# Performance work log

Hardware: AMD Instinct MI355X
Metric: run time of the kernel (lower is better)

The kernel has to match this reference:

```python
import jax, jax.numpy as jnp
import numpy as np

LEAKY_ALPHA = 0.2      # nn.LeakyReLU(alpha)
NEG_FILL = -9e15       # zero_vec fill value
BN_EPS = 1e-5          # BatchNorm1d default eps

N, F_IN, F_OUT, E = 8192, 256, 64, 262144


def setup_inputs() -> dict:
    key = jax.random.key(0)
    ks = jax.random.split(key, 4)
    h = jax.random.normal(ks[0], (N, F_IN), jnp.float32)
    edge_index = jax.random.randint(ks[1], (2, E), 0, N, dtype=jnp.int64)
    # xavier_uniform-scale params
    W = jax.random.normal(ks[2], (F_IN, F_OUT), jnp.float32) * (1.0 / np.sqrt(F_IN))
    a = jax.random.normal(ks[3], (2 * F_OUT, 1), jnp.float32) * 0.1
    bias = jnp.zeros((F_OUT,), jnp.float32)   # filled with 0.0 in reset_parameters0
    gamma = jnp.ones((F_OUT,), jnp.float32)   # BatchNorm1d weight
    beta = jnp.zeros((F_OUT,), jnp.float32)   # BatchNorm1d bias
    return {"h": h, "edge_index": edge_index, "W": W, "a": a,
            "bias": bias, "gamma": gamma, "beta": beta}


def reference(h, edge_index, W, a, bias, gamma, beta):
    # --- GATLayer (num_heads=1, concat=True, activation=None, dropout off) ---
    hp = h @ W                                   # [N, F_OUT]
    n = hp.shape[0]
    f = hp.shape[1]
    # a_input @ a with a_input[i,j] = [hp_i ; hp_j] decomposes as f1_i + f2_j
    a1, a2 = a[:f, 0], a[f:, 0]
    f1 = hp @ a1                                 # [N]
    f2 = hp @ a2                                 # [N]
    e = jax.nn.leaky_relu(f1[:, None] + f2[None, :], LEAKY_ALPHA)  # [N, N]
    row, col = edge_index[0], edge_index[1]
    adj = jnp.zeros((n, n), dtype=bool).at[row, col].set(True)
    att = jax.nn.softmax(jnp.where(adj, e, NEG_FILL), axis=1)      # [N, N]
    alpha = att[row, col]                        # [E]
    out = att @ hp                               # [N, F_OUT]
    # BatchNorm1d, training mode: batch stats, biased variance
    mean = jnp.mean(out, axis=0)
    var = jnp.mean((out - mean) ** 2, axis=0)
    out = (out - mean) / jnp.sqrt(var + BN_EPS) * gamma + beta
    out = out + bias                             # activation is None
    return out, alpha
```

## Files before the change

kernel.cpp:

```cpp
#include <hip/hip_runtime.h>
#include <stdint.h>

#define N_NODES 8192
#define F_IN    256
#define F_OUT   64
#define N_EDGES 262144
#define LEAKY   0.2f
#define BN_EPSF 1e-5f
#define WPR     256
#define MAXDEG  256
#define WT_LD   260
#define SLOTS   8

typedef unsigned int u32;

__device__ __forceinline__ float lrelu(float x) {
    return fmaxf(x, LEAKY * x);
}

__global__ __launch_bounds__(256) void k_pre(
    const float* __restrict__ h, const float* __restrict__ W, const float* __restrict__ a,
    float* __restrict__ hp, float* __restrict__ f1, float* __restrict__ f2,
    u32* __restrict__ bm, float* __restrict__ Sacc)
{
    __shared__ float Wt[F_OUT * WT_LD];
    const int tid = threadIdx.x;
    const int w = tid >> 6, lane = tid & 63;
    const int b = blockIdx.x;

    {
        const float4 z = {0.f, 0.f, 0.f, 0.f};
        float4* dst = reinterpret_cast<float4*>(bm + (size_t)b * 8192);
#pragma unroll
        for (int p = 0; p < 8; ++p) dst[tid + p * 256] = z;
        if (b == 0 && tid < 256)
            reinterpret_cast<float4*>(Sacc)[tid] = z;
    }

#pragma unroll
    for (int t = 0; t < 64; ++t) {
        const int T = t * 4 + w;
        const int o = (T & 7) * 8 + (lane & 7);
        const int k = (T >> 3) * 8 + (lane >> 3);
        Wt[o * WT_LD + k] = W[k * F_OUT + o];
    }
    __syncthreads();

    const int row0 = b * 32;
    const int wu = __builtin_amdgcn_readfirstlane(w);
    const float* hb = h + (size_t)(row0 + wu * 8) * F_IN;
    const int o = lane;

    float acc[8] = {0.f, 0.f, 0.f, 0.f, 0.f, 0.f, 0.f, 0.f};
    for (int q = 0; q < 64; ++q) {
        const float4 wv = *reinterpret_cast<const float4*>(&Wt[o * WT_LD + 4 * q]);
#pragma unroll
        for (int r = 0; r < 8; ++r) {
            const float4 hq = *reinterpret_cast<const float4*>(&hb[r * F_IN + 4 * q]);
            acc[r] += wv.x * hq.x + wv.y * hq.y + wv.z * hq.z + wv.w * hq.w;
        }
    }

    const float a1 = a[o], a2 = a[F_OUT + o];
#pragma unroll
    for (int r = 0; r < 8; ++r) {
        const int row = row0 + wu * 8 + r;
        hp[row * F_OUT + o] = acc[r];
        float p1 = acc[r] * a1;
        float p2 = acc[r] * a2;
#pragma unroll
        for (int off = 32; off; off >>= 1) {
            p1 += __shfl_xor(p1, off, 64);
            p2 += __shfl_xor(p2, off, 64);
        }
        if (o == 0) { f1[row] = p1; f2[row] = p2; }
    }
}

__global__ __launch_bounds__(256) void k_adj(const int* __restrict__ ei, u32* __restrict__ bm)
{
    const int e = blockIdx.x * 256 + threadIdx.x;
    const int r = ei[e];
    const int c = ei[N_EDGES + e];
    atomicOr(&bm[(size_t)r * WPR + (c >> 5)], 1u << (c & 31));
}

__global__ __launch_bounds__(256) void k_attn(
    const u32* __restrict__ bm, const float* __restrict__ hp,
    const float* __restrict__ f1g, const float* __restrict__ f2g,
    float* __restrict__ Mg, float* __restrict__ Dg, float* __restrict__ outr,
    float* __restrict__ Sacc, float* __restrict__ Qacc)
{
    __shared__ int   nbr[4][MAXDEG];
    __shared__ float fv [4][MAXDEG];
    __shared__ float bnS[4][F_OUT], bnQ[4][F_OUT];
    const int tid = threadIdx.x;
    const int w = tid >> 6, lane = tid & 63;
    const int row = blockIdx.x * 4 + w;

    const uint4 bw = reinterpret_cast<const uint4*>(bm + (size_t)row * WPR)[lane];
    const int tot = __popc(bw.x) + __popc(bw.y) + __popc(bw.z) + __popc(bw.w);
    int pref = tot;
#pragma unroll
    for (int off = 1; off < 64; off <<= 1) {
        const int t2 = __shfl_up(pref, off, 64);
        if (lane >= off) pref += t2;
    }
    const int deg0 = __shfl(pref, 63, 64);
    int pos = pref - tot;
    float mymax = -1e30f;
    const u32 words[4] = {bw.x, bw.y, bw.z, bw.w};
    int* nb = nbr[w];
    float* fvv = fv[w];
#pragma unroll
    for (int i = 0; i < 4; ++i) {
        u32 bits = words[i];
        const int jbase = (lane * 4 + i) * 32;
        while (bits) {
            const int bit = __ffs(bits) - 1;
            bits &= bits - 1;
            const int j = jbase + bit;
            const float v = f2g[j];
            mymax = fmaxf(mymax, v);
            if (pos < MAXDEG) { nb[pos] = j; fvv[pos] = v; }
            ++pos;
        }
    }
#pragma unroll
    for (int off = 32; off; off >>= 1)
        mymax = fmaxf(mymax, __shfl_xor(mymax, off, 64));

    const int dg = min(deg0, MAXDEG);
    const float f1i = f1g[row];
    float M = lrelu(f1i + mymax);

    float den0 = 0.f, den1 = 0.f, den2 = 0.f, den3 = 0.f;
    float ac0 = 0.f, ac1 = 0.f, ac2 = 0.f, ac3 = 0.f;
    int n = 0;
    for (; n + 4 <= dg; n += 4) {
        const int j0 = nb[n], j1 = nb[n + 1], j2 = nb[n + 2], j3 = nb[n + 3];
        const float w0 = __expf(lrelu(f1i + fvv[n]) - M);
        const float w1 = __expf(lrelu(f1i + fvv[n + 1]) - M);
        const float w2 = __expf(lrelu(f1i + fvv[n + 2]) - M);
        const float w3 = __expf(lrelu(f1i + fvv[n + 3]) - M);
        den0 += w0; den1 += w1; den2 += w2; den3 += w3;
        ac0 += w0 * hp[j0 * F_OUT + lane];
        ac1 += w1 * hp[j1 * F_OUT + lane];
        ac2 += w2 * hp[j2 * F_OUT + lane];
        ac3 += w3 * hp[j3 * F_OUT + lane];
    }
    for (; n < dg; ++n) {
        const float w0 = __expf(lrelu(f1i + fvv[n]) - M);
        den0 += w0;
        ac0 += w0 * hp[nb[n] * F_OUT + lane];
    }
    float den = (den0 + den1) + (den2 + den3);
    float v = ((ac0 + ac1) + (ac2 + ac3)) / den;
    if (dg == 0) { den = 1.f; M = 0.f; v = 0.f; }

    outr[row * F_OUT + lane] = v;
    if (lane == 0) { Mg[row] = M; Dg[row] = den; }

    bnS[w][lane] = v;
    bnQ[w][lane] = v * v;
    __syncthreads();
    if (w == 0) {
        const float s = bnS[0][lane] + bnS[1][lane] + bnS[2][lane] + bnS[3][lane];
        const float q = bnQ[0][lane] + bnQ[1][lane] + bnQ[2][lane] + bnQ[3][lane];
        const int slot = blockIdx.x & (SLOTS - 1);
        atomicAdd(&Sacc[slot * F_OUT + lane], s);
        atomicAdd(&Qacc[slot * F_OUT + lane], q);
    }
}

__global__ __launch_bounds__(256) void k_post(
    const float* __restrict__ outr, const float* __restrict__ Sacc,
    const float* __restrict__ Qacc, const float* __restrict__ gamma,
    const float* __restrict__ beta, const float* __restrict__ bias,
    const int* __restrict__ ei, const float* __restrict__ f1g,
    const float* __restrict__ f2g, const float* __restrict__ Mg,
    const float* __restrict__ Dg, float* __restrict__ out)
{
    const int tid = threadIdx.x;
    if (blockIdx.x < 512) {
        __shared__ float sm[F_OUT], sr[F_OUT], sg[F_OUT], sb[F_OUT];
        if (tid < F_OUT) {
            float s = 0.f, q = 0.f;
#pragma unroll
            for (int k = 0; k < SLOTS; ++k) {
                s += Sacc[k * F_OUT + tid];
                q += Qacc[k * F_OUT + tid];
            }
            const float mean = s * (1.f / N_NODES);
            const float var = q * (1.f / N_NODES) - mean * mean;
            sm[tid] = mean;
            sr[tid] = rsqrtf(var + BN_EPSF);
            sg[tid] = gamma[tid];
            sb[tid] = beta[tid] + bias[tid];
        }
        __syncthreads();
        const int gid = blockIdx.x * 256 + tid;
        const float4 ov = reinterpret_cast<const float4*>(outr)[gid];
        const int o0 = (gid & 15) * 4;
        float4 res;
        res.x = (ov.x - sm[o0 + 0]) * sr[o0 + 0] * sg[o0 + 0] + sb[o0 + 0];
        res.y = (ov.y - sm[o0 + 1]) * sr[o0 + 1] * sg[o0 + 1] + sb[o0 + 1];
        res.z = (ov.z - sm[o0 + 2]) * sr[o0 + 2] * sg[o0 + 2] + sb[o0 + 2];
        res.w = (ov.w - sm[o0 + 3]) * sr[o0 + 3] * sg[o0 + 3] + sb[o0 + 3];
        reinterpret_cast<float4*>(out)[gid] = res;
    } else {
        const int e = (blockIdx.x - 512) * 256 + tid;
        const int r = ei[e];
        const int c = ei[N_EDGES + e];
        out[N_NODES * F_OUT + e] = __expf(lrelu(f1g[r] + f2g[c]) - Mg[r]) / Dg[r];
    }
}

extern "C" void kernel_launch(void* const* d_in, const int* in_sizes, int n_in,
                              void* d_out, int out_size, void* d_ws, size_t ws_size,
                              hipStream_t stream) {
    const float* h     = (const float*)d_in[0];
    const int*   ei    = (const int*)  d_in[1];
    const float* W     = (const float*)d_in[2];
    const float* a     = (const float*)d_in[3];
    const float* bias  = (const float*)d_in[4];
    const float* gamma = (const float*)d_in[5];
    const float* beta  = (const float*)d_in[6];
    float* out = (float*)d_out;

    char* ws = (char*)d_ws;
    float* hp    = (float*)(ws + 0);
    float* f1    = (float*)(ws + 2097152);
    float* f2    = (float*)(ws + 2129920);
    float* Mg    = (float*)(ws + 2162688);
    float* Dg    = (float*)(ws + 2195456);
    float* outr  = (float*)(ws + 2228224);
    float* Sacc  = (float*)(ws + 4325376);
    float* Qacc  = (float*)(ws + 4327424);
    u32*   bm    = (u32*)  (ws + 4329472);
    if (ws_size < (size_t)4329472 + (size_t)N_NODES * WPR * 4) return;

    k_pre <<<256,  256, 0, stream>>>(h, W, a, hp, f1, f2, bm, Sacc);
    k_adj <<<N_EDGES / 256, 256, 0, stream>>>(ei, bm);
    k_attn<<<N_NODES / 4, 256, 0, stream>>>(bm, hp, f1, f2, Mg, Dg, outr, Sacc, Qacc);
    k_post<<<1536, 256, 0, stream>>>(outr, Sacc, Qacc, gamma, beta, bias,
                                     ei, f1, f2, Mg, Dg, out);
}
```

Measured before the change: 122.2 us.

## Fuse adjacency, attention and BN/alpha passes into one cooperative kernel

Replaces the three launches (adjacency bitmap build, attention aggregation, BN plus alpha output) with one cooperative kernel of 1024 blocks that uses grid.sync between phases. Each block handles 256 edges and 8 rows, two per wavefront. Per-row results stay in registers, so the outr intermediate buffer and its global round trip go away. The cost is two grid-wide barriers, fewer threads doing the neighbour gather with less unrolling, and a dependence on all blocks being co-resident.

After: 322.5 us. 164% more time.

```diff
diff --git a/kernel.cpp b/kernel.cpp
--- a/kernel.cpp
+++ b/kernel.cpp
@@ -1,5 +1,8 @@
 #include <hip/hip_runtime.h>
+#include <hip/hip_cooperative_groups.h>
 #include <stdint.h>
+
+namespace cg = cooperative_groups;
 
 #define N_NODES 8192
 #define F_IN    256
@@ -77,143 +80,125 @@
     }
 }
 
-__global__ __launch_bounds__(256) void k_adj(const int* __restrict__ ei, u32* __restrict__ bm)
-{
-    const int e = blockIdx.x * 256 + threadIdx.x;
-    const int r = ei[e];
-    const int c = ei[N_EDGES + e];
-    atomicOr(&bm[(size_t)r * WPR + (c >> 5)], 1u << (c & 31));
-}
-
-__global__ __launch_bounds__(256) void k_attn(
-    const u32* __restrict__ bm, const float* __restrict__ hp,
+__global__ __launch_bounds__(256, 4) void k_main(
+    const int* __restrict__ ei, const float* __restrict__ hp,
     const float* __restrict__ f1g, const float* __restrict__ f2g,
-    float* __restrict__ Mg, float* __restrict__ Dg, float* __restrict__ outr,
-    float* __restrict__ Sacc, float* __restrict__ Qacc)
+    const float* __restrict__ gamma, const float* __restrict__ beta,
+    const float* __restrict__ bias,
+    u32* __restrict__ bm, float* __restrict__ Mg, float* __restrict__ Dg,
+    float* __restrict__ Sacc, float* __restrict__ Qacc, float* __restrict__ out)
 {
     __shared__ int   nbr[4][MAXDEG];
     __shared__ float fv [4][MAXDEG];
     __shared__ float bnS[4][F_OUT], bnQ[4][F_OUT];
+    __shared__ float fin[4][F_OUT];
+    cg::grid_group grid = cg::this_grid();
     const int tid = threadIdx.x;
     const int w = tid >> 6, lane = tid & 63;
-    const int row = blockIdx.x * 4 + w;
-
-    const uint4 bw = reinterpret_cast<const uint4*>(bm + (size_t)row * WPR)[lane];
-    const int tot = __popc(bw.x) + __popc(bw.y) + __popc(bw.z) + __popc(bw.w);
-    int pref = tot;
-#pragma unroll
-    for (int off = 1; off < 64; off <<= 1) {
-        const int t2 = __shfl_up(pref, off, 64);
-        if (lane >= off) pref += t2;
-    }
-    const int deg0 = __shfl(pref, 63, 64);
-    int pos = pref - tot;
-    float mymax = -1e30f;
-    const u32 words[4] = {bw.x, bw.y, bw.z, bw.w};
+    const int b = blockIdx.x;
+
+    const int e = b * 256 + tid;
+    const int er = ei[e];
+    const int ec = ei[N_EDGES + e];
+    atomicOr(&bm[(size_t)er * WPR + (ec >> 5)], 1u << (ec & 31));
+    grid.sync();
+
+    float vsave[2];
+    float myS = 0.f, myQ = 0.f;
     int* nb = nbr[w];
     float* fvv = fv[w];
 #pragma unroll
-    for (int i = 0; i < 4; ++i) {
-        u32 bits = words[i];
-        const int jbase = (lane * 4 + i) * 32;
-        while (bits) {
-            const int bit = __ffs(bits) - 1;
-            bits &= bits - 1;
-            const int j = jbase + bit;
-            const float v = f2g[j];
-            mymax = fmaxf(mymax, v);
-            if (pos < MAXDEG) { nb[pos] = j; fvv[pos] = v; }
-            ++pos;
-        }
-    }
-#pragma unroll
-    for (int off = 32; off; off >>= 1)
-        mymax = fmaxf(mymax, __shfl_xor(mymax, off, 64));
-
-    const int dg = min(deg0, MAXDEG);
-    const float f1i = f1g[row];
-    float M = lrelu(f1i + mymax);
-
-    float den0 = 0.f, den1 = 0.f, den2 = 0.f, den3 = 0.f;
-    float ac0 = 0.f, ac1 = 0.f, ac2 = 0.f, ac3 = 0.f;
-    int n = 0;
-    for (; n + 4 <= dg; n += 4) {
-        const int j0 = nb[n], j1 = nb[n + 1], j2 = nb[n + 2], j3 = nb[n + 3];
-        const float w0 = __expf(lrelu(f1i + fvv[n]) - M);
-        const float w1 = __expf(lrelu(f1i + fvv[n + 1]) - M);
-        const float w2 = __expf(lrelu(f1i + fvv[n + 2]) - M);
-        const float w3 = __expf(lrelu(f1i + fvv[n + 3]) - M);
-        den0 += w0; den1 += w1; den2 += w2; den3 += w3;
-        ac0 += w0 * hp[j0 * F_OUT + lane];
-        ac1 += w1 * hp[j1 * F_OUT + lane];
-        ac2 += w2 * hp[j2 * F_OUT + lane];
-        ac3 += w3 * hp[j3 * F_OUT + lane];
-    }
-    for (; n < dg; ++n) {
-        const float w0 = __expf(lrelu(f1i + fvv[n]) - M);
-        den0 += w0;
-        ac0 += w0 * hp[nb[n] * F_OUT + lane];
-    }
-    float den = (den0 + den1) + (den2 + den3);
-    float v = ((ac0 + ac1) + (ac2 + ac3)) / den;
-    if (dg == 0) { den = 1.f; M = 0.f; v = 0.f; }
-
-    outr[row * F_OUT + lane] = v;
-    if (lane == 0) { Mg[row] = M; Dg[row] = den; }
-
-    bnS[w][lane] = v;
-    bnQ[w][lane] = v * v;
+    for (int rr = 0; rr < 2; ++rr) {
+        const int row = b * 8 + w * 2 + rr;
+        const uint4 bw = reinterpret_cast<const uint4*>(bm + (size_t)row * WPR)[lane];
+        const int tot = __popc(bw.x) + __popc(bw.y) + __popc(bw.z) + __popc(bw.w);
+        int pref = tot;
+#pragma unroll
+        for (int off = 1; off < 64; off <<= 1) {
+            const int t2 = __shfl_up(pref, off, 64);
+            if (lane >= off) pref += t2;
+        }
+        const int deg0 = __shfl(pref, 63, 64);
+        int pos = pref - tot;
+        float mymax = -1e30f;
+        const u32 words[4] = {bw.x, bw.y, bw.z, bw.w};
+#pragma unroll
+        for (int i = 0; i < 4; ++i) {
+            u32 bits = words[i];
+            const int jbase = (lane * 4 + i) * 32;
+            while (bits) {
+                const int bit = __ffs(bits) - 1;
+                bits &= bits - 1;
+                const int j = jbase + bit;
+                const float v = f2g[j];
+                mymax = fmaxf(mymax, v);
+                if (pos < MAXDEG) { nb[pos] = j; fvv[pos] = v; }
+                ++pos;
+            }
+        }
+#pragma unroll
+        for (int off = 32; off; off >>= 1)
+            mymax = fmaxf(mymax, __shfl_xor(mymax, off, 64));
+
+        const int dg = min(deg0, MAXDEG);
+        const float f1i = f1g[row];
+        float M = lrelu(f1i + mymax);
+        float den0 = 0.f, den1 = 0.f, ac0 = 0.f, ac1 = 0.f;
+        int n = 0;
+        for (; n + 2 <= dg; n += 2) {
+            const int j0 = nb[n], j1 = nb[n + 1];
+            const float w0 = __expf(lrelu(f1i + fvv[n]) - M);
+            const float w1 = __expf(lrelu(f1i + fvv[n + 1]) - M);
+            den0 += w0;  den1 += w1;
+            ac0 += w0 * hp[j0 * F_OUT + lane];
+            ac1 += w1 * hp[j1 * F_OUT + lane];
+        }
+        if (n < dg) {
+            const float w0 = __expf(lrelu(f1i + fvv[n]) - M);
+            den0 += w0;
+            ac0 += w0 * hp[nb[n] * F_OUT + lane];
+        }
+        float den = den0 + den1;
+        float v = (ac0 + ac1) / den;
+        if (dg == 0) { den = 1.f; M = 0.f; v = 0.f; }
+        vsave[rr] = v;
+        myS += v; myQ += v * v;
+        if (lane == 0) { Mg[row] = M; Dg[row] = den; }
+    }
+    bnS[w][lane] = myS;
+    bnQ[w][lane] = myQ;
     __syncthreads();
     if (w == 0) {
         const float s = bnS[0][lane] + bnS[1][lane] + bnS[2][lane] + bnS[3][lane];
         const float q = bnQ[0][lane] + bnQ[1][lane] + bnQ[2][lane] + bnQ[3][lane];
-        const int slot = blockIdx.x & (SLOTS - 1);
+        const int slot = b & (SLOTS - 1);
         atomicAdd(&Sacc[slot * F_OUT + lane], s);
         atomicAdd(&Qacc[slot * F_OUT + lane], q);
     }
-}
-
-__global__ __launch_bounds__(256) void k_post(
-    const float* __restrict__ outr, const float* __restrict__ Sacc,
-    const float* __restrict__ Qacc, const float* __restrict__ gamma,
-    const float* __restrict__ beta, const float* __restrict__ bias,
-    const int* __restrict__ ei, const float* __restrict__ f1g,
-    const float* __restrict__ f2g, const float* __restrict__ Mg,
-    const float* __restrict__ Dg, float* __restrict__ out)
-{
-    const int tid = threadIdx.x;
-    if (blockIdx.x < 512) {
-        __shared__ float sm[F_OUT], sr[F_OUT], sg[F_OUT], sb[F_OUT];
-        if (tid < F_OUT) {
-            float s = 0.f, q = 0.f;
-#pragma unroll
-            for (int k = 0; k < SLOTS; ++k) {
-                s += Sacc[k * F_OUT + tid];
-                q += Qacc[k * F_OUT + tid];
-            }
-            const float mean = s * (1.f / N_NODES);
-            const float var = q * (1.f / N_NODES) - mean * mean;
-            sm[tid] = mean;
-            sr[tid] = rsqrtf(var + BN_EPSF);
-            sg[tid] = gamma[tid];
-            sb[tid] = beta[tid] + bias[tid];
-        }
-        __syncthreads();
-        const int gid = blockIdx.x * 256 + tid;
-        const float4 ov = reinterpret_cast<const float4*>(outr)[gid];
-        const int o0 = (gid & 15) * 4;
-        float4 res;
-        res.x = (ov.x - sm[o0 + 0]) * sr[o0 + 0] * sg[o0 + 0] + sb[o0 + 0];
-        res.y = (ov.y - sm[o0 + 1]) * sr[o0 + 1] * sg[o0 + 1] + sb[o0 + 1];
-        res.z = (ov.z - sm[o0 + 2]) * sr[o0 + 2] * sg[o0 + 2] + sb[o0 + 2];
-        res.w = (ov.w - sm[o0 + 3]) * sr[o0 + 3] * sg[o0 + 3] + sb[o0 + 3];
-        reinterpret_cast<float4*>(out)[gid] = res;
-    } else {
-        const int e = (blockIdx.x - 512) * 256 + tid;
-        const int r = ei[e];
-        const int c = ei[N_EDGES + e];
-        out[N_NODES * F_OUT + e] = __expf(lrelu(f1g[r] + f2g[c]) - Mg[r]) / Dg[r];
-    }
+    grid.sync();
+
+    if (tid < F_OUT) {
+        float s = 0.f, q = 0.f;
+#pragma unroll
+        for (int k = 0; k < SLOTS; ++k) {
+            s += Sacc[k * F_OUT + tid];
+            q += Qacc[k * F_OUT + tid];
+        }
+        const float mean = s * (1.f / N_NODES);
+        const float var = q * (1.f / N_NODES) - mean * mean;
+        fin[0][tid] = mean;
+        fin[1][tid] = rsqrtf(var + BN_EPSF);
+        fin[2][tid] = gamma[tid];
+        fin[3][tid] = beta[tid] + bias[tid];
+    }
+    __syncthreads();
+#pragma unroll
+    for (int rr = 0; rr < 2; ++rr) {
+        const int row = b * 8 + w * 2 + rr;
+        out[row * F_OUT + lane] =
+            (vsave[rr] - fin[0][lane]) * fin[1][lane] * fin[2][lane] + fin[3][lane];
+    }
+    out[N_NODES * F_OUT + e] = __expf(lrelu(f1g[er] + f2g[ec]) - Mg[er]) / Dg[er];
 }
 
 extern "C" void kernel_launch(void* const* d_in, const int* in_sizes, int n_in,
@@ -234,15 +219,16 @@
     float* f2    = (float*)(ws + 2129920);
     float* Mg    = (float*)(ws + 2162688);
     float* Dg    = (float*)(ws + 2195456);
-    float* outr  = (float*)(ws + 2228224);
-    float* Sacc  = (float*)(ws + 4325376);
-    float* Qacc  = (float*)(ws + 4327424);
-    u32*   bm    = (u32*)  (ws + 4329472);
-    if (ws_size < (size_t)4329472 + (size_t)N_NODES * WPR * 4) return;
-
-    k_pre <<<256,  256, 0, stream>>>(h, W, a, hp, f1, f2, bm, Sacc);
-    k_adj <<<N_EDGES / 256, 256, 0, stream>>>(ei, bm);
-    k_attn<<<N_NODES / 4, 256, 0, stream>>>(bm, hp, f1, f2, Mg, Dg, outr, Sacc, Qacc);
-    k_post<<<1536, 256, 0, stream>>>(outr, Sacc, Qacc, gamma, beta, bias,
-                                     ei, f1, f2, Mg, Dg, out);
-}
+    float* Sacc  = (float*)(ws + 2228224);
+    float* Qacc  = (float*)(ws + 2230272);
+    u32*   bm    = (u32*)  (ws + 2232320);
+    if (ws_size < (size_t)2232320 + (size_t)N_NODES * WPR * 4) return;
+
+    k_pre<<<256, 256, 0, stream>>>(h, W, a, hp, f1, f2, bm, Sacc);
+
+    void* args[] = {(void*)&ei, (void*)&hp, (void*)&f1, (void*)&f2,
+                    (void*)&gamma, (void*)&beta, (void*)&bias,
+                    (void*)&bm, (void*)&Mg, (void*)&Dg,
+                    (void*)&Sacc, (void*)&Qacc, (void*)&out};
+    hipLaunchCooperativeKernel((void*)k_main, dim3(1024), dim3(256), args, 0, stream);
+}
```

## Replace dense adjacency bitmap with per-row edge lists and fuse alpha output

Applied to the files above, without the earlier changes.

Edges are now bucketed into per-row lists using atomic counters, inside the projection kernel. This removes the 8 MB bitmap zero-fill, the atomicOr build pass and the 256-word bitmap scan per row. Duplicate edges are removed with a small shared-memory bitmap per wave, and alpha is scattered straight from the attention kernel. That drops the separate per-edge pass and the M/D/outr temporaries, and the BatchNorm pass now normalises the output in place. The costs are global atomic contention on the row counters, a hard cap of 256 neighbours per row, and per-lane arrays indexed by a runtime loop bound, which may spill to scratch.

Result: faster. 116.2 us (-5.0%).

```diff
diff --git a/kernel.cpp b/kernel.cpp
--- a/kernel.cpp
+++ b/kernel.cpp
@@ -7,35 +7,38 @@
 #define N_EDGES 262144
 #define LEAKY   0.2f
 #define BN_EPSF 1e-5f
-#define WPR     256
 #define MAXDEG  256
 #define WT_LD   260
 #define SLOTS   8
 
 typedef unsigned int u32;
+typedef unsigned long long u64;
 
 __device__ __forceinline__ float lrelu(float x) {
     return fmaxf(x, LEAKY * x);
 }
 
-__global__ __launch_bounds__(256) void k_pre(
+__global__ __launch_bounds__(256) void k_gs(
     const float* __restrict__ h, const float* __restrict__ W, const float* __restrict__ a,
+    const int* __restrict__ ei,
     float* __restrict__ hp, float* __restrict__ f1, float* __restrict__ f2,
-    u32* __restrict__ bm, float* __restrict__ Sacc)
+    u32* __restrict__ cnt, u32* __restrict__ elist)
 {
     __shared__ float Wt[F_OUT * WT_LD];
     const int tid = threadIdx.x;
+
+    if (blockIdx.x >= 256) {
+        const int e = (blockIdx.x - 256) * 256 + tid;
+        const int r = ei[e];
+        const int c = ei[N_EDGES + e];
+        const int pos = atomicAdd(&cnt[r], 1u);
+        if (pos < MAXDEG)
+            elist[r * MAXDEG + pos] = ((u32)e << 13) | (u32)c;
+        return;
+    }
+
     const int w = tid >> 6, lane = tid & 63;
     const int b = blockIdx.x;
-
-    {
-        const float4 z = {0.f, 0.f, 0.f, 0.f};
-        float4* dst = reinterpret_cast<float4*>(bm + (size_t)b * 8192);
-#pragma unroll
-        for (int p = 0; p < 8; ++p) dst[tid + p * 256] = z;
-        if (b == 0 && tid < 256)
-            reinterpret_cast<float4*>(Sacc)[tid] = z;
-    }
 
 #pragma unroll
     for (int t = 0; t < 64; ++t) {
@@ -77,89 +80,84 @@
     }
 }
 
-__global__ __launch_bounds__(256) void k_adj(const int* __restrict__ ei, u32* __restrict__ bm)
+__global__ __launch_bounds__(256) void k_attn(
+    const u32* __restrict__ cnt, const u32* __restrict__ elist,
+    const float* __restrict__ hp, const float* __restrict__ f1g,
+    const float* __restrict__ f2g,
+    float* __restrict__ Sacc, float* __restrict__ Qacc, float* __restrict__ out)
 {
-    const int e = blockIdx.x * 256 + threadIdx.x;
-    const int r = ei[e];
-    const int c = ei[N_EDGES + e];
-    atomicOr(&bm[(size_t)r * WPR + (c >> 5)], 1u << (c & 31));
-}
-
-__global__ __launch_bounds__(256) void k_attn(
-    const u32* __restrict__ bm, const float* __restrict__ hp,
-    const float* __restrict__ f1g, const float* __restrict__ f2g,
-    float* __restrict__ Mg, float* __restrict__ Dg, float* __restrict__ outr,
-    float* __restrict__ Sacc, float* __restrict__ Qacc)
-{
-    __shared__ int   nbr[4][MAXDEG];
-    __shared__ float fv [4][MAXDEG];
+    __shared__ u32   dbm[4][256];
     __shared__ float bnS[4][F_OUT], bnQ[4][F_OUT];
     const int tid = threadIdx.x;
     const int w = tid >> 6, lane = tid & 63;
     const int row = blockIdx.x * 4 + w;
 
-    const uint4 bw = reinterpret_cast<const uint4*>(bm + (size_t)row * WPR)[lane];
-    const int tot = __popc(bw.x) + __popc(bw.y) + __popc(bw.z) + __popc(bw.w);
-    int pref = tot;
-#pragma unroll
-    for (int off = 1; off < 64; off <<= 1) {
-        const int t2 = __shfl_up(pref, off, 64);
-        if (lane >= off) pref += t2;
-    }
-    const int deg0 = __shfl(pref, 63, 64);
-    int pos = pref - tot;
+    const int dg = min((int)cnt[row], MAXDEG);
+    const float f1i = f1g[row];
+    const int nch = (dg + 63) >> 6;
+
+    {
+        const uint4 z = {0u, 0u, 0u, 0u};
+        reinterpret_cast<uint4*>(dbm[w])[lane] = z;
+    }
+
+    int   cc[4]; u32 ee[4]; float vv[4];
     float mymax = -1e30f;
-    const u32 words[4] = {bw.x, bw.y, bw.z, bw.w};
-    int* nb = nbr[w];
-    float* fvv = fv[w];
-#pragma unroll
-    for (int i = 0; i < 4; ++i) {
-        u32 bits = words[i];
-        const int jbase = (lane * 4 + i) * 32;
-        while (bits) {
-            const int bit = __ffs(bits) - 1;
-            bits &= bits - 1;
-            const int j = jbase + bit;
-            const float v = f2g[j];
-            mymax = fmaxf(mymax, v);
-            if (pos < MAXDEG) { nb[pos] = j; fvv[pos] = v; }
-            ++pos;
-        }
+#pragma unroll 4
+    for (int k = 0; k < nch; ++k) {
+        const int idx = k * 64 + lane;
+        const u32 pv = (idx < dg) ? elist[row * MAXDEG + idx] : 0u;
+        cc[k] = pv & 8191u;
+        ee[k] = pv >> 13;
+        vv[k] = (idx < dg) ? f2g[cc[k]] : -1e30f;
+        mymax = fmaxf(mymax, vv[k]);
     }
 #pragma unroll
     for (int off = 32; off; off >>= 1)
         mymax = fmaxf(mymax, __shfl_xor(mymax, off, 64));
-
-    const int dg = min(deg0, MAXDEG);
-    const float f1i = f1g[row];
-    float M = lrelu(f1i + mymax);
-
-    float den0 = 0.f, den1 = 0.f, den2 = 0.f, den3 = 0.f;
-    float ac0 = 0.f, ac1 = 0.f, ac2 = 0.f, ac3 = 0.f;
-    int n = 0;
-    for (; n + 4 <= dg; n += 4) {
-        const int j0 = nb[n], j1 = nb[n + 1], j2 = nb[n + 2], j3 = nb[n + 3];
-        const float w0 = __expf(lrelu(f1i + fvv[n]) - M);
-        const float w1 = __expf(lrelu(f1i + fvv[n + 1]) - M);
-        const float w2 = __expf(lrelu(f1i + fvv[n + 2]) - M);
-        const float w3 = __expf(lrelu(f1i + fvv[n + 3]) - M);
-        den0 += w0; den1 += w1; den2 += w2; den3 += w3;
-        ac0 += w0 * hp[j0 * F_OUT + lane];
-        ac1 += w1 * hp[j1 * F_OUT + lane];
-        ac2 += w2 * hp[j2 * F_OUT + lane];
-        ac3 += w3 * hp[j3 * F_OUT + lane];
-    }
-    for (; n < dg; ++n) {
-        const float w0 = __expf(lrelu(f1i + fvv[n]) - M);
-        den0 += w0;
-        ac0 += w0 * hp[nb[n] * F_OUT + lane];
-    }
-    float den = (den0 + den1) + (den2 + den3);
-    float v = ((ac0 + ac1) + (ac2 + ac3)) / den;
-    if (dg == 0) { den = 1.f; M = 0.f; v = 0.f; }
-
-    outr[row * F_OUT + lane] = v;
-    if (lane == 0) { Mg[row] = M; Dg[row] = den; }
+    const float M = lrelu(f1i + mymax);
+
+    float wgt[4]; u64 keep[4];
+    float den = 0.f;
+#pragma unroll 4
+    for (int k = 0; k < nch; ++k) {
+        const int idx = k * 64 + lane;
+        bool kp = false;
+        wgt[k] = 0.f;
+        if (idx < dg) {
+            const u32 bit = 1u << (cc[k] & 31);
+            const u32 old = atomicOr(&dbm[w][cc[k] >> 5], bit);
+            kp = !(old & bit);
+            wgt[k] = __expf(lrelu(f1i + vv[k]) - M);
+        }
+        keep[k] = __ballot(kp);
+        den += kp ? wgt[k] : 0.f;
+    }
+#pragma unroll
+    for (int off = 32; off; off >>= 1)
+        den += __shfl_xor(den, off, 64);
+
+    float acc = 0.f;
+#pragma unroll 4
+    for (int k = 0; k < nch; ++k) {
+        u64 m = keep[k];
+        while (m) {
+            const int n = __ffsll((unsigned long long)m) - 1;
+            m &= m - 1;
+            const int j = __shfl(cc[k], n, 64);
+            const float wn = __shfl(wgt[k], n, 64);
+            acc += wn * hp[j * F_OUT + lane];
+        }
+    }
+    float v = (dg == 0) ? 0.f : acc / den;
+    out[row * F_OUT + lane] = v;
+
+#pragma unroll 4
+    for (int k = 0; k < nch; ++k) {
+        const int idx = k * 64 + lane;
+        if (idx < dg)
+            out[N_NODES * F_OUT + ee[k]] = wgt[k] / den;
+    }
 
     bnS[w][lane] = v;
     bnQ[w][lane] = v * v;
@@ -173,47 +171,37 @@
     }
 }
 
-__global__ __launch_bounds__(256) void k_post(
-    const float* __restrict__ outr, const float* __restrict__ Sacc,
-    const float* __restrict__ Qacc, const float* __restrict__ gamma,
-    const float* __restrict__ beta, const float* __restrict__ bias,
-    const int* __restrict__ ei, const float* __restrict__ f1g,
-    const float* __restrict__ f2g, const float* __restrict__ Mg,
-    const float* __restrict__ Dg, float* __restrict__ out)
+__global__ __launch_bounds__(256) void k_bn(
+    const float* __restrict__ Sacc, const float* __restrict__ Qacc,
+    const float* __restrict__ gamma, const float* __restrict__ beta,
+    const float* __restrict__ bias, float* __restrict__ out)
 {
+    __shared__ float sm[F_OUT], sr[F_OUT], sg[F_OUT], sb[F_OUT];
     const int tid = threadIdx.x;
-    if (blockIdx.x < 512) {
-        __shared__ float sm[F_OUT], sr[F_OUT], sg[F_OUT], sb[F_OUT];
-        if (tid < F_OUT) {
-            float s = 0.f, q = 0.f;
-#pragma unroll
-            for (int k = 0; k < SLOTS; ++k) {
-                s += Sacc[k * F_OUT + tid];
-                q += Qacc[k * F_OUT + tid];
-            }
-            const float mean = s * (1.f / N_NODES);
-            const float var = q * (1.f / N_NODES) - mean * mean;
-            sm[tid] = mean;
-            sr[tid] = rsqrtf(var + BN_EPSF);
-            sg[tid] = gamma[tid];
-            sb[tid] = beta[tid] + bias[tid];
-        }
-        __syncthreads();
-        const int gid = blockIdx.x * 256 + tid;
-        const float4 ov = reinterpret_cast<const float4*>(outr)[gid];
-        const int o0 = (gid & 15) * 4;
-        float4 res;
-        res.x = (ov.x - sm[o0 + 0]) * sr[o0 + 0] * sg[o0 + 0] + sb[o0 + 0];
-        res.y = (ov.y - sm[o0 + 1]) * sr[o0 + 1] * sg[o0 + 1] + sb[o0 + 1];
-        res.z = (ov.z - sm[o0 + 2]) * sr[o0 + 2] * sg[o0 + 2] + sb[o0 + 2];
-        res.w = (ov.w - sm[o0 + 3]) * sr[o0 + 3] * sg[o0 + 3] + sb[o0 + 3];
-        reinterpret_cast<float4*>(out)[gid] = res;
-    } else {
-        const int e = (blockIdx.x - 512) * 256 + tid;
-        const int r = ei[e];
-        const int c = ei[N_EDGES + e];
-        out[N_NODES * F_OUT + e] = __expf(lrelu(f1g[r] + f2g[c]) - Mg[r]) / Dg[r];
-    }
+    if (tid < F_OUT) {
+        float s = 0.f, q = 0.f;
+#pragma unroll
+        for (int k = 0; k < SLOTS; ++k) {
+            s += Sacc[k * F_OUT + tid];
+            q += Qacc[k * F_OUT + tid];
+        }
+        const float mean = s * (1.f / N_NODES);
+        const float var = q * (1.f / N_NODES) - mean * mean;
+        sm[tid] = mean;
+        sr[tid] = rsqrtf(var + BN_EPSF);
+        sg[tid] = gamma[tid];
+        sb[tid] = beta[tid] + bias[tid];
+    }
+    __syncthreads();
+    const int gid = blockIdx.x * 256 + tid;
+    const float4 ov = reinterpret_cast<const float4*>(out)[gid];
+    const int o0 = (gid & 15) * 4;
+    float4 res;
+    res.x = (ov.x - sm[o0 + 0]) * sr[o0 + 0] * sg[o0 + 0] + sb[o0 + 0];
+    res.y = (ov.y - sm[o0 + 1]) * sr[o0 + 1] * sg[o0 + 1] + sb[o0 + 1];
+    res.z = (ov.z - sm[o0 + 2]) * sr[o0 + 2] * sg[o0 + 2] + sb[o0 + 2];
+    res.w = (ov.w - sm[o0 + 3]) * sr[o0 + 3] * sg[o0 + 3] + sb[o0 + 3];
+    reinterpret_cast<float4*>(out)[gid] = res;
 }
 
 extern "C" void kernel_launch(void* const* d_in, const int* in_sizes, int n_in,
@@ -229,20 +217,19 @@
     float* out = (float*)d_out;
 
     char* ws = (char*)d_ws;
-    float* hp    = (float*)(ws + 0);
-    float* f1    = (float*)(ws + 2097152);
-    float* f2    = (float*)(ws + 2129920);
-    float* Mg    = (float*)(ws + 2162688);
-    float* Dg    = (float*)(ws + 2195456);
-    float* outr  = (float*)(ws + 2228224);
-    float* Sacc  = (float*)(ws + 4325376);
-    float* Qacc  = (float*)(ws + 4327424);
-    u32*   bm    = (u32*)  (ws + 4329472);
-    if (ws_size < (size_t)4329472 + (size_t)N_NODES * WPR * 4) return;
-
-    k_pre <<<256,  256, 0, stream>>>(h, W, a, hp, f1, f2, bm, Sacc);
-    k_adj <<<N_EDGES / 256, 256, 0, stream>>>(ei, bm);
-    k_attn<<<N_NODES / 4, 256, 0, stream>>>(bm, hp, f1, f2, Mg, Dg, outr, Sacc, Qacc);
-    k_post<<<1536, 256, 0, stream>>>(outr, Sacc, Qacc, gamma, beta, bias,
-                                     ei, f1, f2, Mg, Dg, out);
-}
+    u32*   cnt   = (u32*)  (ws + 0);
+    float* Sacc  = (float*)(ws + 32768);
+    float* Qacc  = (float*)(ws + 34816);
+    float* hp    = (float*)(ws + 36864);
+    float* f1    = (float*)(ws + 2134016);
+    float* f2    = (float*)(ws + 2166784);
+    u32*   elist = (u32*)  (ws + 2199552);
+    if (ws_size < (size_t)2199552 + (size_t)N_NODES * MAXDEG * 4) return;
+
+    hipMemsetAsync(ws, 0, 36864, stream);
+    k_gs  <<<1280, 256, 0, stream>>>(h, W, a, ei, hp, f1, f2, cnt, elist);
+    k_attn<<<N_NODES / 4, 256, 0, stream>>>(cnt, elist, hp, f1, f2,
+                                            Sacc, Qacc, out);
+    k_bn  <<<(N_NODES * F_OUT) / 1024, 256, 0, stream>>>(Sacc, Qacc, gamma,
+                                                         beta, bias, out);
+}
```
